# Optimization experiments

Hardware: AMD Instinct MI355X
Metric: run time of the kernel (lower is better)

The kernel has to match this reference:

```python
import jax, jax.numpy as jnp
import numpy as np

B, S, E, H, V, G = 32, 2048, 300, 256, 50000, 5


def setup_inputs() -> dict:
    key = jax.random.key(0)
    ks = jax.random.split(key, 12)
    return {
        "token_ids": jax.random.randint(ks[0], (B, S), 0, V),
        "emb": jax.random.normal(ks[1], (V, E), jnp.float32) * 0.1,
        "W_ih_f": jax.random.normal(ks[2], (H, E), jnp.float32) * 0.05,
        "W_hh_f": jax.random.normal(ks[3], (H, H), jnp.float32) * 0.05,
        "b_ih_f": jax.random.normal(ks[4], (H,), jnp.float32) * 0.05,
        "b_hh_f": jax.random.normal(ks[5], (H,), jnp.float32) * 0.05,
        "W_ih_b": jax.random.normal(ks[6], (H, E), jnp.float32) * 0.05,
        "W_hh_b": jax.random.normal(ks[7], (H, H), jnp.float32) * 0.05,
        "b_ih_b": jax.random.normal(ks[8], (H,), jnp.float32) * 0.05,
        "b_hh_b": jax.random.normal(ks[9], (H,), jnp.float32) * 0.05,
        "fc_W": jax.random.normal(ks[10], (G, 2 * H), jnp.float32) * 0.05,
        "fc_b": jax.random.normal(ks[11], (G,), jnp.float32) * 0.05,
    }


def _rnn_dir(x_tm, W_ih, W_hh, b_ih, b_hh):
    # x_tm: [S, B, E] time-major. Precompute input projection once (GEMM),
    # then scan only the recurrent part. h_t = tanh(x W_ih^T + b_ih + h W_hh^T + b_hh)
    xproj = jnp.einsum('sbe,he->sbh', x_tm, W_ih) + b_ih + b_hh  # [S,B,H]
    h0 = jnp.zeros((x_tm.shape[1], W_hh.shape[0]), x_tm.dtype)

    def step(h, xp):
        h_new = jnp.tanh(xp + h @ W_hh.T)
        return h_new, h_new

    _, hs = jax.lax.scan(step, h0, xproj)
    return hs  # [S, B, H]


def reference(token_ids, emb, W_ih_f, W_hh_f, b_ih_f, b_hh_f,
              W_ih_b, W_hh_b, b_ih_b, b_hh_b, fc_W, fc_b):
    x = emb[token_ids]                      # [B, S, E] embedding lookup
    x_tm = jnp.swapaxes(x, 0, 1)            # [S, B, E]
    hs_f = _rnn_dir(x_tm, W_ih_f, W_hh_f, b_ih_f, b_hh_f)          # forward dir
    hs_b = _rnn_dir(x_tm[::-1], W_ih_b, W_hh_b, b_ih_b, b_hh_b)[::-1]  # backward dir
    out_seq = jnp.concatenate([hs_f, hs_b], axis=-1)  # [S, B, 2H]
    # MoT_layer: mean over time (vectorized form of the nested-loop mean)
    pooled = jnp.mean(out_seq, axis=0)      # [B, 2H]
    # dropout (eval / identity), then activation, then fc
    act = jnp.tanh(pooled)
    return act @ fc_W.T + fc_b              # [B, G]
```

## Files before the change

### kernel.cpp

```cpp
#include <hip/hip_runtime.h>
#include <hip/hip_bf16.h>

#define S_LEN 2048
#define BB 32
#define EE 300
#define HH 256
#define VV 50000
#define GG 5

#define K2LOG2E 2.8853900817779268f

typedef float f32x4 __attribute__((ext_vector_type(4)));
typedef float f32x2 __attribute__((ext_vector_type(2)));
typedef __bf16 bf16x8 __attribute__((ext_vector_type(8)));
typedef int i32x4 __attribute__((ext_vector_type(4)));

__device__ __forceinline__ unsigned short f2bf(float f) {
    unsigned int u = __builtin_bit_cast(unsigned int, f);
    u = u + 0x7fffu + ((u >> 16) & 1u);
    return (unsigned short)(u >> 16);
}
__device__ __forceinline__ float bflo(unsigned int w) {
    return __builtin_bit_cast(float, w << 16);
}
__device__ __forceinline__ float bfhi(unsigned int w) {
    return __builtin_bit_cast(float, w & 0xffff0000u);
}
__device__ __forceinline__ float tanh_pre(float xs) {
    float e = __builtin_amdgcn_exp2f(xs);
    float r = __builtin_amdgcn_rcpf(e + 1.0f);
    return __builtin_fmaf(-2.0f, r, 1.0f);
}
__device__ __forceinline__ float tanhf_fast(float x) {
    return tanh_pre(x * K2LOG2E);
}
__device__ __forceinline__ unsigned int cvt_pk_bf16(float lo, float hi) {
    unsigned int r;
    asm("v_cvt_pk_bf16_f32 %0, %1, %2" : "=v"(r) : "v"(lo), "v"(hi));
    return r;
}
__device__ __forceinline__ f32x2 pk_add(f32x2 a, f32x2 b) {
    f32x2 d;
    asm("v_pk_add_f32 %0, %1, %2" : "=v"(d) : "v"(a), "v"(b));
    return d;
}

__global__ void k_pack(const float* __restrict__ Wih_f, const float* __restrict__ Whh_f,
                       const float* __restrict__ bih_f, const float* __restrict__ bhh_f,
                       const float* __restrict__ Wih_b, const float* __restrict__ Whh_b,
                       const float* __restrict__ bih_b, const float* __restrict__ bhh_b,
                       unsigned short* __restrict__ Wp, unsigned short* __restrict__ Whp,
                       float* __restrict__ biasc)
{
    int idx = blockIdx.x * 256 + threadIdx.x;
    if (idx < 163840) {
        int i = idx & 7, j = (idx >> 3) & 255, kg = (idx >> 11) & 3, kbd = idx >> 13;
        int kb = kbd % 10, dir = kbd / 10;
        int e = kb * 32 + kg * 8 + i;
        const float* W = dir ? Wih_b : Wih_f;
        float v = (e < EE) ? W[j * EE + e] * K2LOG2E : 0.0f;
        Wp[idx] = f2bf(v);
    } else if (idx < 163840 + 131072) {
        int x = idx - 163840;
        int i = x & 7, j = (x >> 3) & 255, kg = (x >> 11) & 3, kbd = x >> 13;
        int kb = kbd & 7, dir = kbd >> 3;
        int k = kb * 32 + kg * 8 + i;
        const float* W = dir ? Whh_b : Whh_f;
        Whp[x] = f2bf(W[j * HH + k] * K2LOG2E);
    } else if (idx < 163840 + 131072 + 512) {
        int x = idx - (163840 + 131072);
        int j = x & 255, dir = x >> 8;
        biasc[x] = (dir ? (bih_b[j] + bhh_b[j]) : (bih_f[j] + bhh_f[j])) * K2LOG2E;
    }
}

__global__ __launch_bounds__(1024) void k_xproj(
    const int* __restrict__ tok, const float* __restrict__ emb,
    const unsigned short* __restrict__ Wp, const float* __restrict__ biasc,
    unsigned short* __restrict__ xq)
{
    __shared__ char xs[32 * 640];
    int s = blockIdx.x;
    int tid = threadIdx.x;
    int lane = tid & 63, W16 = tid >> 6;

    #pragma unroll
    for (int k = 0; k < 5; k++) ((int*)xs)[tid + k * 1024] = 0;
    __syncthreads();

    {
        int b0 = W16 * 2;
        for (int rr = 0; rr < 2; rr++) {
            int b = b0 + rr;
            int t = tok[b * S_LEN + s];
            const float* row = emb + (size_t)t * EE;
            int xorv = (b & 7) << 4;
            #pragma unroll
            for (int c = 0; c < 5; c++) {
                int e = c * 64 + lane;
                if (e < EE) {
                    *(unsigned short*)(xs + b * 640 + ((2 * e) ^ xorv)) = f2bf(row[e]);
                }
            }
        }
    }
    __syncthreads();

    int dir = W16 >> 3, w = (W16 >> 1) & 3, half = W16 & 1;
    int l15 = lane & 15, kg = lane >> 4;
    f32x4 acc[4] = {};
    int brow = half * 16 + l15;
    int bxor = (brow & 7) << 4;
    const char* xrow = xs + brow * 640;

    #pragma unroll
    for (int kb = 0; kb < 10; kb++) {
        bf16x8 xb = *(const bf16x8*)(xrow + ((kb * 64 + kg * 16) ^ bxor));
        #pragma unroll
        for (int t = 0; t < 4; t++) {
            int j = w * 64 + t * 16 + l15;
            bf16x8 wa = *(const bf16x8*)(Wp + (size_t)(((dir * 10 + kb) * 4 + kg) * 256 + j) * 8);
            acc[t] = __builtin_amdgcn_mfma_f32_16x16x32_bf16(wa, xb, acc[t], 0, 0, 0);
        }
    }

    unsigned int words[8];
    #pragma unroll
    for (int t = 0; t < 4; t++) {
        float v[4];
        #pragma unroll
        for (int r = 0; r < 4; r++) {
            int j = w * 64 + t * 16 + kg * 4 + r;
            v[r] = acc[t][r] + biasc[dir * 256 + j];
        }
        words[t * 2 + 0] = cvt_pk_bf16(v[0], v[1]);
        words[t * 2 + 1] = cvt_pk_bf16(v[2], v[3]);
    }
    size_t base = (size_t)s * 32768 + (size_t)((dir * 2 + half) * 4 + w) * 2048 + (size_t)lane * 32;
    *(i32x4*)((char*)xq + base) = *(i32x4*)&words[0];
    *(i32x4*)((char*)xq + base + 16) = *(i32x4*)&words[4];
}

__global__ __launch_bounds__(512, 2) void k_rnn(
    const unsigned short* __restrict__ xq,
    const unsigned short* __restrict__ Whp,
    float* __restrict__ pooled)
{
    __shared__ char hb0[8192];
    __shared__ char hb1[8192];
    int bid = blockIdx.x;
    int dir = bid >> 1, half = bid & 1;
    int tid = threadIdx.x;
    int lane = tid & 63, w = tid >> 6;
    int l15 = lane & 15, kg = lane >> 4;

    bf16x8 wf0[8], wf1[8];
    #pragma unroll
    for (int kb = 0; kb < 8; kb++) {
        int jbase = (((dir * 8 + kb) * 4 + kg) * 256 + w * 32 + l15);
        wf0[kb] = *(const bf16x8*)(Whp + (size_t)jbase * 8);
        wf1[kb] = *(const bf16x8*)(Whp + (size_t)(jbase + 16) * 8);
    }

    *(i32x4*)(&hb0[tid * 16]) = i32x4{0, 0, 0, 0};

    f32x2 px[4] = {};

    int rbase = kg * 256 + l15 * 16;
    int woff0 = w * 1024 + (kg >> 1) * 256 + l15 * 16 + (kg & 1) * 8;
    int woff1 = woff0 + 512;

    int lanebase = ((dir * 2 + half) * 4 + (w >> 1)) * 2048 + lane * 32 + (w & 1) * 16;
    int sdelta = dir ? -32768 : 32768;
    int s0 = dir ? (S_LEN - 1) : 0;

    const char* xqb = (const char*)xq;
    int xoff = s0 * 32768 + lanebase;
    i32x4 xc0 = *(const i32x4*)(xqb + xoff); xoff += sdelta;
    i32x4 xc1 = *(const i32x4*)(xqb + xoff); xoff += sdelta;

    __syncthreads();

#define STEP(RB, WB, XC, DO_PF)                                                      \
    {                                                                                \
        const char* rb = (RB) + rbase;                                               \
        bf16x8 hf[8];                                                                \
        _Pragma("unroll")                                                            \
        for (int kb = 0; kb < 8; kb++)                                               \
            hf[kb] = *(const bf16x8*)(rb + kb * 1024);                               \
        f32x4 acc0, acc1;                                                            \
        acc0[0] = bflo((unsigned int)XC[0]);                                         \
        acc0[1] = bfhi((unsigned int)XC[0]);                                         \
        acc0[2] = bflo((unsigned int)XC[1]);                                         \
        acc0[3] = bfhi((unsigned int)XC[1]);                                         \
        acc1[0] = bflo((unsigned int)XC[2]);                                         \
        acc1[1] = bfhi((unsigned int)XC[2]);                                         \
        acc1[2] = bflo((unsigned int)XC[3]);                                         \
        acc1[3] = bfhi((unsigned int)XC[3]);                                         \
        if (DO_PF) { XC = *(const i32x4*)(xqb + xoff); xoff += sdelta; }             \
        _Pragma("unroll")                                                            \
        for (int kb = 0; kb < 8; kb++) {                                             \
            acc0 = __builtin_amdgcn_mfma_f32_16x16x32_bf16(wf0[kb], hf[kb],          \
                                                           acc0, 0, 0, 0);           \
            acc1 = __builtin_amdgcn_mfma_f32_16x16x32_bf16(wf1[kb], hf[kb],          \
                                                           acc1, 0, 0, 0);           \
        }                                                                            \
        float h0 = tanh_pre(acc0[0]);                                                \
        float h1 = tanh_pre(acc0[1]);                                                \
        float h2 = tanh_pre(acc0[2]);                                                \
        float h3 = tanh_pre(acc0[3]);                                                \
        float h4 = tanh_pre(acc1[0]);                                                \
        float h5 = tanh_pre(acc1[1]);                                                \
        float h6 = tanh_pre(acc1[2]);                                                \
        float h7 = tanh_pre(acc1[3]);                                                \
        *(uint2*)((WB) + woff0) = make_uint2(cvt_pk_bf16(h0, h1),                    \
                                             cvt_pk_bf16(h2, h3));                   \
        *(uint2*)((WB) + woff1) = make_uint2(cvt_pk_bf16(h4, h5),                    \
                                             cvt_pk_bf16(h6, h7));                   \
        asm volatile("s_waitcnt lgkmcnt(0)" ::: "memory");                           \
        __builtin_amdgcn_s_barrier();                                                \
        px[0] = pk_add(px[0], f32x2{h0, h1});                                        \
        px[1] = pk_add(px[1], f32x2{h2, h3});                                        \
        px[2] = pk_add(px[2], f32x2{h4, h5});                                        \
        px[3] = pk_add(px[3], f32x2{h6, h7});                                        \
    }

    for (int i = 0; i < S_LEN - 4; i += 2) {
        STEP(hb0, hb1, xc0, 1)
        STEP(hb1, hb0, xc1, 1)
    }
    STEP(hb0, hb1, xc0, 1)
    STEP(hb1, hb0, xc1, 1)
    STEP(hb0, hb1, xc0, 0)
    STEP(hb1, hb0, xc1, 0)
#undef STEP

    #pragma unroll
    for (int q = 0; q < 2; q++)
        #pragma unroll
        for (int r = 0; r < 4; r++) {
            int j = w * 32 + q * 16 + kg * 4 + r;
            int b = half * 16 + l15;
            pooled[b * 512 + dir * 256 + j] = px[q * 2 + (r >> 1)][r & 1];
        }
}

__global__ __launch_bounds__(64) void k_head(
    const float* __restrict__ pooled, const float* __restrict__ fcW,
    const float* __restrict__ fcb, float* __restrict__ out)
{
    int b = blockIdx.x;
    int lane = threadIdx.x;
    float p[GG] = {0, 0, 0, 0, 0};
    for (int jj = lane; jj < 512; jj += 64) {
        float a = tanhf_fast(pooled[b * 512 + jj] * (1.0f / 2048.0f));
        #pragma unroll
        for (int g = 0; g < GG; g++) p[g] += a * fcW[g * 512 + jj];
    }
    #pragma unroll
    for (int g = 0; g < GG; g++)
        #pragma unroll
        for (int off = 32; off; off >>= 1) p[g] += __shfl_xor(p[g], off);
    if (lane == 0) {
        #pragma unroll
        for (int g = 0; g < GG; g++) out[b * GG + g] = p[g] + fcb[g];
    }
}

extern "C" void kernel_launch(void* const* d_in, const int* in_sizes, int n_in,
                              void* d_out, int out_size, void* d_ws, size_t ws_size,
                              hipStream_t stream)
{
    const int* tok = (const int*)d_in[0];
    const float* emb = (const float*)d_in[1];
    const float* Wih_f = (const float*)d_in[2];
    const float* Whh_f = (const float*)d_in[3];
    const float* bih_f = (const float*)d_in[4];
    const float* bhh_f = (const float*)d_in[5];
    const float* Wih_b = (const float*)d_in[6];
    const float* Whh_b = (const float*)d_in[7];
    const float* bih_b = (const float*)d_in[8];
    const float* bhh_b = (const float*)d_in[9];
    const float* fcW = (const float*)d_in[10];
    const float* fcb = (const float*)d_in[11];
    float* out = (float*)d_out;

    char* ws = (char*)d_ws;
    unsigned short* xq   = (unsigned short*)(ws);
    unsigned short* Wp   = (unsigned short*)(ws + 67108864);
    unsigned short* Whp  = (unsigned short*)(ws + 67108864 + 327680);
    float* biasc         = (float*)(ws + 67108864 + 327680 + 262144);
    float* pooled        = (float*)(ws + 67108864 + 327680 + 262144 + 2048);

    hipLaunchKernelGGL(k_pack, dim3(1154), dim3(256), 0, stream,
                       Wih_f, Whh_f, bih_f, bhh_f, Wih_b, Whh_b, bih_b, bhh_b,
                       Wp, Whp, biasc);
    hipLaunchKernelGGL(k_xproj, dim3(2048), dim3(1024), 0, stream,
                       tok, emb, Wp, biasc, xq);
    hipLaunchKernelGGL(k_rnn, dim3(4), dim3(512), 0, stream, xq, Whp, pooled);
    hipLaunchKernelGGL(k_head, dim3(32), dim3(64), 0, stream, pooled, fcW, fcb, out);
}
```

Before: 1.158 ms.

## Split RNN recurrent work across 12 waves with uneven tile ownership

The recurrent kernel goes from 8 waves, each owning two 16-row output tiles, to 12 waves in 4 groups of 3. In each group one wave keeps two tiles and the other two handle one tile each, which shortens the per-step critical path for most waves. The two-tile wave gets higher scheduling priority, since it now sets the pace of each barrier step. The cost is more waves joining every per-step barrier and an imbalance, because the two-tile wave still does twice the MFMA work.

```diff
diff --git a/kernel.cpp b/kernel.cpp
--- a/kernel.cpp
+++ b/kernel.cpp
@@ -141,7 +141,7 @@
     *(i32x4*)((char*)xq + base + 16) = *(i32x4*)&words[4];
 }
 
-__global__ __launch_bounds__(512, 2) void k_rnn(
+__global__ __launch_bounds__(768, 3) void k_rnn(
     const unsigned short* __restrict__ xq,
     const unsigned short* __restrict__ Whp,
     float* __restrict__ pooled)
@@ -153,35 +153,37 @@
     int tid = threadIdx.x;
     int lane = tid & 63, w = tid >> 6;
     int l15 = lane & 15, kg = lane >> 4;
-
-    bf16x8 wf0[8], wf1[8];
-    #pragma unroll
-    for (int kb = 0; kb < 8; kb++) {
-        int jbase = (((dir * 8 + kb) * 4 + kg) * 256 + w * 32 + l15);
-        wf0[kb] = *(const bf16x8*)(Whp + (size_t)jbase * 8);
-        wf1[kb] = *(const bf16x8*)(Whp + (size_t)(jbase + 16) * 8);
-    }
-
-    *(i32x4*)(&hb0[tid * 16]) = i32x4{0, 0, 0, 0};
-
-    f32x2 px[4] = {};
+    int g = w / 3, r = w % 3;
+
+    if (tid < 512) *(i32x4*)(&hb0[tid * 16]) = i32x4{0, 0, 0, 0};
 
     int rbase = kg * 256 + l15 * 16;
-    int woff0 = w * 1024 + (kg >> 1) * 256 + l15 * 16 + (kg & 1) * 8;
-    int woff1 = woff0 + 512;
-
-    int lanebase = ((dir * 2 + half) * 4 + (w >> 1)) * 2048 + lane * 32 + (w & 1) * 16;
+#define WOFF(t) (((t) >> 1) * 1024 + (((t) & 1) * 2 + (kg >> 1)) * 256 + l15 * 16 + (kg & 1) * 8)
+
     int sdelta = dir ? -32768 : 32768;
     int s0 = dir ? (S_LEN - 1) : 0;
-
     const char* xqb = (const char*)xq;
-    int xoff = s0 * 32768 + lanebase;
-    i32x4 xc0 = *(const i32x4*)(xqb + xoff); xoff += sdelta;
-    i32x4 xc1 = *(const i32x4*)(xqb + xoff); xoff += sdelta;
+    int xrec = ((dir * 2 + half) * 4 + g) * 2048 + lane * 32;
 
     __syncthreads();
 
-#define STEP(RB, WB, XC, DO_PF)                                                      \
+    if (r == 0) {
+        int t0 = 4 * g, t1 = 4 * g + 1;
+        bf16x8 wf0[8], wf1[8];
+        #pragma unroll
+        for (int kb = 0; kb < 8; kb++) {
+            int jb = ((dir * 8 + kb) * 4 + kg) * 256;
+            wf0[kb] = *(const bf16x8*)(Whp + (size_t)(jb + t0 * 16 + l15) * 8);
+            wf1[kb] = *(const bf16x8*)(Whp + (size_t)(jb + t1 * 16 + l15) * 8);
+        }
+        int woff0 = WOFF(t0), woff1 = WOFF(t1);
+        int xoff = s0 * 32768 + xrec;
+        i32x4 xc0 = *(const i32x4*)(xqb + xoff); xoff += sdelta;
+        i32x4 xc1 = *(const i32x4*)(xqb + xoff); xoff += sdelta;
+        f32x2 px[4] = {};
+        __builtin_amdgcn_s_setprio(1);
+
+#define STEP2(RB, WB, XC, DO_PF)                                                     \
     {                                                                                \
         const char* rb = (RB) + rbase;                                               \
         bf16x8 hf[8];                                                                \
@@ -225,24 +227,81 @@
         px[3] = pk_add(px[3], f32x2{h6, h7});                                        \
     }
 
-    for (int i = 0; i < S_LEN - 4; i += 2) {
-        STEP(hb0, hb1, xc0, 1)
-        STEP(hb1, hb0, xc1, 1)
-    }
-    STEP(hb0, hb1, xc0, 1)
-    STEP(hb1, hb0, xc1, 1)
-    STEP(hb0, hb1, xc0, 0)
-    STEP(hb1, hb0, xc1, 0)
-#undef STEP
-
-    #pragma unroll
-    for (int q = 0; q < 2; q++)
-        #pragma unroll
-        for (int r = 0; r < 4; r++) {
-            int j = w * 32 + q * 16 + kg * 4 + r;
-            int b = half * 16 + l15;
-            pooled[b * 512 + dir * 256 + j] = px[q * 2 + (r >> 1)][r & 1];
-        }
+        for (int i = 0; i < S_LEN - 4; i += 2) {
+            STEP2(hb0, hb1, xc0, 1)
+            STEP2(hb1, hb0, xc1, 1)
+        }
+        STEP2(hb0, hb1, xc0, 1)
+        STEP2(hb1, hb0, xc1, 1)
+        STEP2(hb0, hb1, xc0, 0)
+        STEP2(hb1, hb0, xc1, 0)
+#undef STEP2
+
+        int b = half * 16 + l15;
+        #pragma unroll
+        for (int rr = 0; rr < 4; rr++) {
+            pooled[b * 512 + dir * 256 + t0 * 16 + kg * 4 + rr] = px[rr >> 1][rr & 1];
+            pooled[b * 512 + dir * 256 + t1 * 16 + kg * 4 + rr] = px[2 + (rr >> 1)][rr & 1];
+        }
+    } else {
+        int t = 4 * g + 1 + r;
+        bf16x8 wf[8];
+        #pragma unroll
+        for (int kb = 0; kb < 8; kb++) {
+            int jb = ((dir * 8 + kb) * 4 + kg) * 256;
+            wf[kb] = *(const bf16x8*)(Whp + (size_t)(jb + t * 16 + l15) * 8);
+        }
+        int woff = WOFF(t);
+        int xoff = s0 * 32768 + xrec + (r + 1) * 8;
+        uint2 xc0 = *(const uint2*)(xqb + xoff); xoff += sdelta;
+        uint2 xc1 = *(const uint2*)(xqb + xoff); xoff += sdelta;
+        f32x2 px[2] = {};
+
+#define STEP1(RB, WB, XC, DO_PF)                                                     \
+    {                                                                                \
+        const char* rb = (RB) + rbase;                                               \
+        bf16x8 hf[8];                                                                \
+        _Pragma("unroll")                                                            \
+        for (int kb = 0; kb < 8; kb++)                                               \
+            hf[kb] = *(const bf16x8*)(rb + kb * 1024);                               \
+        f32x4 acc;                                                                   \
+        acc[0] = bflo(XC.x);                                                         \
+        acc[1] = bfhi(XC.x);                                                         \
+        acc[2] = bflo(XC.y);                                                         \
+        acc[3] = bfhi(XC.y);                                                         \
+        if (DO_PF) { XC = *(const uint2*)(xqb + xoff); xoff += sdelta; }             \
+        _Pragma("unroll")                                                            \
+        for (int kb = 0; kb < 8; kb++)                                               \
+            acc = __builtin_amdgcn_mfma_f32_16x16x32_bf16(wf[kb], hf[kb],            \
+                                                          acc, 0, 0, 0);             \
+        float h0 = tanh_pre(acc[0]);                                                 \
+        float h1 = tanh_pre(acc[1]);                                                 \
+        float h2 = tanh_pre(acc[2]);                                                 \
+        float h3 = tanh_pre(acc[3]);                                                 \
+        *(uint2*)((WB) + woff) = make_uint2(cvt_pk_bf16(h0, h1),                     \
+                                            cvt_pk_bf16(h2, h3));                    \
+        asm volatile("s_waitcnt lgkmcnt(0)" ::: "memory");                           \
+        __builtin_amdgcn_s_barrier();                                                \
+        px[0] = pk_add(px[0], f32x2{h0, h1});                                        \
+        px[1] = pk_add(px[1], f32x2{h2, h3});                                        \
+    }
+
+        for (int i = 0; i < S_LEN - 4; i += 2) {
+            STEP1(hb0, hb1, xc0, 1)
+            STEP1(hb1, hb0, xc1, 1)
+        }
+        STEP1(hb0, hb1, xc0, 1)
+        STEP1(hb1, hb0, xc1, 1)
+        STEP1(hb0, hb1, xc0, 0)
+        STEP1(hb1, hb0, xc1, 0)
+#undef STEP1
+
+        int b = half * 16 + l15;
+        #pragma unroll
+        for (int rr = 0; rr < 4; rr++)
+            pooled[b * 512 + dir * 256 + t * 16 + kg * 4 + rr] = px[rr >> 1][rr & 1];
+    }
+#undef WOFF
 }
 
 __global__ __launch_bounds__(64) void k_head(
@@ -297,6 +356,6 @@
                        Wp, Whp, biasc);
     hipLaunchKernelGGL(k_xproj, dim3(2048), dim3(1024), 0, stream,
                        tok, emb, Wp, biasc, xq);
-    hipLaunchKernelGGL(k_rnn, dim3(4), dim3(512), 0, stream, xq, Whp, pooled);
+    hipLaunchKernelGGL(k_rnn, dim3(4), dim3(768), 0, stream, xq, Whp, pooled);
     hipLaunchKernelGGL(k_head, dim3(32), dim3(64), 0, stream, pooled, fcW, fcb, out);
 }
```

After: 1.091 ms. -5.8%, faster.
